# Optimization experiments

Measured on AMD Instinct MI355X. Metric: run time of the kernel, lower is better.

Reference implementation:

```python
import jax, jax.numpy as jnp
import numpy as np

HID = 64
NUM_LAYERS = 2
EPS = 1e-5


def _layernorm(x, g, b):
    mu = jnp.mean(x, axis=-1, keepdims=True)
    var = jnp.mean(jnp.square(x - mu), axis=-1, keepdims=True)
    return (x - mu) * jax.lax.rsqrt(var + EPS) * g + b


def _mlp(x, w1, b1, g, beta, w2, b2):
    # Linear -> LayerNorm -> ReLU -> Linear (torch Linear: x @ W.T + b)
    h = x @ w1.T + b1
    h = jax.nn.relu(_layernorm(h, g, beta))
    return h @ w2.T + b2


def _gru(x, h, wih, whh, bih, bhh):
    # PyTorch GRUCell semantics
    gi = x @ wih.T + bih
    gh = h @ whh.T + bhh
    ir, iz, inn = jnp.split(gi, 3, axis=-1)
    hr, hz, hn = jnp.split(gh, 3, axis=-1)
    r = jax.nn.sigmoid(ir + hr)
    z = jax.nn.sigmoid(iz + hz)
    n = jnp.tanh(inn + r * hn)
    return (1.0 - z) * n + z * h


def setup_inputs() -> dict:
    key = jax.random.key(0)
    ks = iter(jax.random.split(key, 64))
    s = 0.05

    def rn(shape):
        return jax.random.normal(next(ks), shape, dtype=jnp.float32) * s

    B, M, K1 = 32, 256, 128
    inp = {
        'hybrid_input': jax.random.normal(next(ks), (B, M, K1, 4), dtype=jnp.float32),
        'hidden_state': jnp.zeros((B, HID), dtype=jnp.float32),
        # input encoder
        'enc_w1': rn((HID, 4)), 'enc_b1': rn((HID,)),
        'enc_g': jnp.ones((HID,), jnp.float32), 'enc_beta': jnp.zeros((HID,), jnp.float32),
        'enc_w2': rn((HID, HID)), 'enc_b2': rn((HID,)),
        # per-layer, per-side (axis0=layer, axis1=[row,col]) params
        'l_w1': rn((NUM_LAYERS, 2, HID, HID)), 'l_b1': rn((NUM_LAYERS, 2, HID)),
        'l_g': jnp.ones((NUM_LAYERS, 2, HID), jnp.float32), 'l_beta': jnp.zeros((NUM_LAYERS, 2, HID), jnp.float32),
        'l_w2': rn((NUM_LAYERS, 2, HID, HID)), 'l_b2': rn((NUM_LAYERS, 2, HID)),
        'l_gwih': rn((NUM_LAYERS, 2, 3 * HID, HID)), 'l_gwhh': rn((NUM_LAYERS, 2, 3 * HID, HID)),
        'l_gbih': rn((NUM_LAYERS, 2, 3 * HID)), 'l_gbhh': rn((NUM_LAYERS, 2, 3 * HID)),
        # top-level GRU
        'g_wih': rn((3 * HID, HID)), 'g_whh': rn((3 * HID, HID)),
        'g_bih': rn((3 * HID,)), 'g_bhh': rn((3 * HID,)),
        # head: Linear(2H->H) -> ReLU -> Linear(H->1)
        'head_w1': rn((HID, 2 * HID)), 'head_b1': rn((HID,)),
        'head_w2': rn((1, HID)), 'head_b2': rn((1,)),
    }
    return inp


def reference(hybrid_input, hidden_state, enc_w1, enc_b1, enc_g, enc_beta, enc_w2, enc_b2,
              l_w1, l_b1, l_g, l_beta, l_w2, l_b2, l_gwih, l_gwhh, l_gbih, l_gbhh,
              g_wih, g_whh, g_bih, g_bhh, head_w1, head_b1, head_w2, head_b2):
    # input encoder
    x = _mlp(hybrid_input, enc_w1, enc_b1, enc_g, enc_beta, enc_w2, enc_b2)

    for l in range(NUM_LAYERS):
        # row pass: max over axis 2 (K+1)
        row_max = jnp.max(x, axis=2, keepdims=True)
        upd = _mlp(x - row_max, l_w1[l, 0], l_b1[l, 0], l_g[l, 0], l_beta[l, 0], l_w2[l, 0], l_b2[l, 0])
        x = _gru(upd, x, l_gwih[l, 0], l_gwhh[l, 0], l_gbih[l, 0], l_gbhh[l, 0])
        # col pass: max over axis 1 (M)
        col_max = jnp.max(x, axis=1, keepdims=True)
        upd = _mlp(x - col_max, l_w1[l, 1], l_b1[l, 1], l_g[l, 1], l_beta[l, 1], l_w2[l, 1], l_b2[l, 1])
        x = _gru(upd, x, l_gwih[l, 1], l_gwhh[l, 1], l_gbih[l, 1], l_gbhh[l, 1])

    B, M, K1, h = x.shape
    global_feat = jnp.max(x.reshape(B, M * K1, h), axis=1)  # (B, H)
    new_hidden = _gru(global_feat, hidden_state, g_wih, g_whh, g_bih, g_bhh)

    h_exp = jnp.broadcast_to(new_hidden[:, None, None, :], (B, M, K1, h))
    combined = jnp.concatenate([x, h_exp], axis=-1)  # (B, M, K1, 2H)
    hh = jax.nn.relu(combined @ head_w1.T + head_b1)
    logits = (hh @ head_w2.T + head_b2)[..., 0]  # (B, M, K1)
    return logits, new_hidden
```

## Files before the change

kernel.cpp:

```cpp
#include <hip/hip_runtime.h>
#include <math.h>

typedef unsigned int u32;
typedef unsigned short u16;
typedef __attribute__((ext_vector_type(4))) float f32x4;
typedef __attribute__((ext_vector_type(8))) short s16x8;

#define NTOT 1048576
#define SWZ(n, col) ((col) ^ (((n) & 7) << 4))

__device__ __forceinline__ float bflo(u32 v) { return __uint_as_float(v << 16); }
__device__ __forceinline__ float bfhi(u32 v) { return __uint_as_float(v & 0xffff0000u); }
__device__ __forceinline__ u16 f2bf(float f) {
  u32 u = __float_as_uint(f);
  u32 r = ((u >> 16) & 1u) + 0x7fffu;
  return (u16)((u + r) >> 16);
}
__device__ __forceinline__ u32 pk2(float a, float b) {
  return (u32)f2bf(a) | ((u32)f2bf(b) << 16);
}
__device__ __forceinline__ float sigm(float x) {
  return __builtin_amdgcn_rcpf(1.0f + __expf(-x));
}
__device__ __forceinline__ float tanh_f(float x) {
  float e = __expf(2.0f * x);
  return 1.0f - 2.0f * __builtin_amdgcn_rcpf(e + 1.0f);
}
__device__ __forceinline__ float relu(float x) { return fmaxf(x, 0.0f); }

__device__ __forceinline__ void gemmG(const ushort* __restrict__ gA,
                                      const unsigned char* L, int boff,
                                      int ws, int l, int lq, int lr,
                                      f32x4 acc[4]) {
  s16x8 a0 = *(const s16x8*)(gA + ((ws * 128 + l) << 3));
  s16x8 a1 = *(const s16x8*)(gA + ((ws * 128 + 64 + l) << 3));
  const int c0 = (lq << 4) ^ ((lr & 7) << 4);
  const unsigned char* Bp = L + boff + lr * 128;
#pragma unroll
  for (int nt = 0; nt < 4; ++nt) {
    s16x8 b0 = *(const s16x8*)(Bp + nt * 2048 + c0);
    s16x8 b1 = *(const s16x8*)(Bp + nt * 2048 + (c0 ^ 64));
    acc[nt] = __builtin_amdgcn_mfma_f32_16x16x32_bf16(a0, b0, acc[nt], 0, 0, 0);
    acc[nt] = __builtin_amdgcn_mfma_f32_16x16x32_bf16(a1, b1, acc[nt], 0, 0, 0);
  }
}

__device__ __forceinline__ void gemmG2(const ushort* __restrict__ gA,
                                       const unsigned char* L, int boff,
                                       int ws, int nh, int l, int lq, int lr,
                                       f32x4 acc[4]) {
  s16x8 a0 = *(const s16x8*)(gA + ((ws * 128 + l) << 3));
  s16x8 a1 = *(const s16x8*)(gA + ((ws * 128 + 64 + l) << 3));
  const int c0 = (lq << 4) ^ ((lr & 7) << 4);
  const unsigned char* Bp = L + boff + nh * 8192 + lr * 128;
#pragma unroll
  for (int nt = 0; nt < 4; ++nt) {
    s16x8 b0 = *(const s16x8*)(Bp + nt * 2048 + c0);
    s16x8 b1 = *(const s16x8*)(Bp + nt * 2048 + (c0 ^ 64));
    acc[nt] = __builtin_amdgcn_mfma_f32_16x16x32_bf16(a0, b0, acc[nt], 0, 0, 0);
    acc[nt] = __builtin_amdgcn_mfma_f32_16x16x32_bf16(a1, b1, acc[nt], 0, 0, 0);
  }
}

__device__ __forceinline__ void binit(f32x4 acc[4], float x, float y, float z, float w) {
  f32x4 v; v[0] = x; v[1] = y; v[2] = z; v[3] = w;
#pragma unroll
  for (int nt = 0; nt < 4; ++nt) acc[nt] = v;
}

__global__ void diag_kernel(float* out, float v) { out[0] = v; }

__global__ __launch_bounds__(256) void prep_kernel(
    const float* __restrict__ enc_w2, const float* __restrict__ head_w1,
    const float* __restrict__ l_w1, const float* __restrict__ l_w2,
    const float* __restrict__ l_gwih, const float* __restrict__ l_gwhh,
    ushort* __restrict__ gwF) {
  const int id = blockIdx.x;
  const int t = threadIdx.x;
  const float* src;
  int ld = 64;
  if (id == 0)      { src = enc_w2; }
  else if (id == 1) { src = head_w1; ld = 128; }
  else if (id < 6)  { src = l_w1 + (id - 2) * 4096; }
  else if (id < 10) { src = l_w2 + (id - 6) * 4096; }
  else if (id < 22) { int q = id - 10; src = l_gwih + (q / 3) * 12288 + (q % 3) * 4096; }
  else              { int q = id - 22; src = l_gwhh + (q / 3) * 12288 + (q % 3) * 4096; }
  uint4* dst = (uint4*)(gwF + (size_t)id * 4096);
#pragma unroll
  for (int i = 0; i < 2; ++i) {
    int ch = i * 256 + t;
    int q = ch & 63;
    int g = ch >> 6;
    int j = (g >> 1) * 16 + (q & 15);
    int k = (g & 1) * 32 + (q >> 4) * 8;
    const float* s = src + (size_t)j * ld + k;
    float4 f0 = *(const float4*)(s);
    float4 f1 = *(const float4*)(s + 4);
    uint4 o;
    o.x = pk2(f0.x, f0.y); o.y = pk2(f0.z, f0.w);
    o.z = pk2(f1.x, f1.y); o.w = pk2(f1.z, f1.w);
    dst[ch] = o;
  }
}

__global__ __launch_bounds__(512) void encoder_kernel(
    const float4* __restrict__ hyb, ushort* __restrict__ xG,
    const ushort* __restrict__ gwF, const float* __restrict__ enc_w1,
    const float* __restrict__ b1, const float* __restrict__ gg,
    const float* __restrict__ be, const float* __restrict__ b2,
    float* __restrict__ rmOut) {
  __shared__ __align__(16) unsigned char L[34304];
  const int t = threadIdx.x;
  const int w = t >> 6, l = t & 63, lq = l >> 4, lr = l & 15;
  const int ws = w & 3, nh = w >> 2;
  const int gbase = blockIdx.x * 128;
  const int j0 = ws * 16 + lq * 4;
  const int colb = ws * 32 + lq * 8;

  if (t < 256) ((float*)(L + 32768))[t] = enc_w1[t];
  __syncthreads();

  {
    const int n = t >> 2, part = t & 3;
    float4 iv = hyb[gbase + n];
    const float* W1 = (const float*)(L + 32768);
    float h[16];
#pragma unroll
    for (int jj = 0; jj < 16; ++jj) {
      int j = part * 16 + jj;
      float4 wr = *(const float4*)(W1 + j * 4);
      h[jj] = b1[j] + wr.x * iv.x + wr.y * iv.y + wr.z * iv.z + wr.w * iv.w;
    }
    float s = 0.f, q = 0.f;
#pragma unroll
    for (int jj = 0; jj < 16; ++jj) { s += h[jj]; q += h[jj] * h[jj]; }
    s += __shfl_xor(s, 1); q += __shfl_xor(q, 1);
    s += __shfl_xor(s, 2); q += __shfl_xor(q, 2);
    float mean = s * (1.f / 64.f);
    float rstd = rsqrtf(q * (1.f / 64.f) - mean * mean + 1e-5f);
    u32 pk[8];
#pragma unroll
    for (int jj = 0; jj < 16; jj += 2) {
      int j = part * 16 + jj;
      float v0 = relu((h[jj] - mean) * rstd * gg[j] + be[j]);
      float v1 = relu((h[jj + 1] - mean) * rstd * gg[j + 1] + be[j + 1]);
      pk[jj >> 1] = pk2(v0, v1);
    }
    *(uint4*)(L + n * 128 + SWZ(n, part * 32))      = make_uint4(pk[0], pk[1], pk[2], pk[3]);
    *(uint4*)(L + n * 128 + SWZ(n, part * 32 + 16)) = make_uint4(pk[4], pk[5], pk[6], pk[7]);
  }
  __syncthreads();

  float4 vb2 = *(const float4*)(b2 + j0);
  f32x4 acc[4];
  binit(acc, vb2.x, vb2.y, vb2.z, vb2.w);
  gemmG2(gwF, L, 0, ws, nh, l, lq, lr, acc);
#pragma unroll
  for (int nt = 0; nt < 4; ++nt) {
    int n = nh * 64 + nt * 16 + lr;
    *(uint2*)(L + 16384 + n * 128 + SWZ(n, colb)) =
        make_uint2(pk2(acc[nt][0], acc[nt][1]), pk2(acc[nt][2], acc[nt][3]));
  }
  {
    float mt[4];
#pragma unroll
    for (int r = 0; r < 4; ++r)
      mt[r] = fmaxf(fmaxf(acc[0][r], acc[1][r]), fmaxf(acc[2][r], acc[3][r]));
#pragma unroll
    for (int m = 1; m < 16; m <<= 1)
#pragma unroll
      for (int r = 0; r < 4; ++r) mt[r] = fmaxf(mt[r], __shfl_xor(mt[r], m));
    if (lr == 0) {
      float4 v; v.x = mt[0]; v.y = mt[1]; v.z = mt[2]; v.w = mt[3];
      *(float4*)(L + 33792 + (nh * 64 + j0) * 4) = v;
    }
  }
  __syncthreads();
  {
    uint4* xout = (uint4*)(xG + (size_t)gbase * 64);
#pragma unroll
    for (int i = 0; i < 2; ++i) {
      int flat = i * 512 + t; int n = flat >> 3, c = flat & 7;
      xout[(size_t)n * 8 + c] = *(const uint4*)(L + 16384 + n * 128 + SWZ(n, c * 16));
    }
  }
  if (t < 64) {
    const float* R = (const float*)(L + 33792);
    float v = fmaxf(R[t], R[64 + t]);
    rmOut[(size_t)(blockIdx.x * 2 + 0) * 64 + t] = v;
    rmOut[(size_t)(blockIdx.x * 2 + 1) * 64 + t] = v;
  }
}

#define PXL 0
#define PP  8192
#define PRED 16384

__global__ __launch_bounds__(256, 4) void pass_kernel(
    ushort* __restrict__ xG, const ushort* __restrict__ gwF,
    const float* __restrict__ rmP, const float* __restrict__ cmG, int mode,
    int s_w1, int s_w2, int s_ih0, int s_hh0,
    const float* __restrict__ b1, const float* __restrict__ b2,
    const float* __restrict__ gg, const float* __restrict__ be,
    const float* __restrict__ bih, const float* __restrict__ bhh,
    float* __restrict__ rmOut) {
  __shared__ __align__(16) unsigned char L[18432];
  const int t = threadIdx.x;
  const int ws = t >> 6, l = t & 63, lq = l >> 4, lr = l & 15;
  const int gbase = blockIdx.x * 64;
  const int j0 = ws * 16 + lq * 4;
  const int colb = ws * 32 + lq * 8;
  const int rowp = (gbase >> 7) * 2;
  const int b = gbase >> 15;
  const int k1b = gbase & 127;

  const ushort* Aw1 = gwF + (size_t)s_w1 * 4096;
  const ushort* Aw2 = gwF + (size_t)s_w2 * 4096;
  const ushort* Ai0 = gwF + (size_t)s_ih0 * 4096;
  const ushort* Ai1 = Ai0 + 4096;
  const ushort* Ai2 = Ai1 + 4096;
  const ushort* Ah0 = gwF + (size_t)s_hh0 * 4096;
  const ushort* Ah1 = Ah0 + 4096;
  const ushort* Ah2 = Ah1 + 4096;

  {
    const uint4* xrow = (const uint4*)(xG + (size_t)gbase * 64);
#pragma unroll
    for (int i = 0; i < 2; ++i) {
      int flat = i * 256 + t; int n = flat >> 3, c = flat & 7;
      uint4 xv = xrow[(size_t)n * 8 + c];
      *(uint4*)(L + PXL + n * 128 + SWZ(n, c * 16)) = xv;
      float mv[8];
      if (mode == 0) {
        const float* r0 = rmP + (size_t)rowp * 64 + c * 8;
#pragma unroll
        for (int q = 0; q < 8; ++q) mv[q] = fmaxf(r0[q], r0[64 + q]);
      } else {
        const float* cp = cmG + ((size_t)(b * 128 + k1b + n)) * 64 + c * 8;
#pragma unroll
        for (int q = 0; q < 8; ++q) mv[q] = cp[q];
      }
      uint4 o;
      o.x = pk2(bflo(xv.x) - mv[0], bfhi(xv.x) - mv[1]);
      o.y = pk2(bflo(xv.y) - mv[2], bfhi(xv.y) - mv[3]);
      o.z = pk2(bflo(xv.z) - mv[4], bfhi(xv.z) - mv[5]);
      o.w = pk2(bflo(xv.w) - mv[6], bfhi(xv.w) - mv[7]);
      *(uint4*)(L + PP + n * 128 + SWZ(n, c * 16)) = o;
    }
  }
  __syncthreads();

  f32x4 acc[4];
  { float4 v = *(const float4*)(b1 + j0); binit(acc, v.x, v.y, v.z, v.w); }
  gemmG(Aw1, L, PP, ws, l, lq, lr, acc);
#pragma unroll
  for (int nt = 0; nt < 4; ++nt) {
    float s = acc[nt][0] + acc[nt][1] + acc[nt][2] + acc[nt][3];
    float q = acc[nt][0] * acc[nt][0] + acc[nt][1] * acc[nt][1] +
              acc[nt][2] * acc[nt][2] + acc[nt][3] * acc[nt][3];
    s += __shfl_xor(s, 16); q += __shfl_xor(q, 16);
    s += __shfl_xor(s, 32); q += __shfl_xor(q, 32);
    if (lq == 0)
      *(float2*)(L + PRED + (ws * 64 + nt * 16 + lr) * 8) = make_float2(s, q);
  }
  __syncthreads();
  {
    float4 vg = *(const float4*)(gg + j0);
    float4 vbe = *(const float4*)(be + j0);
    float gv[4] = {vg.x, vg.y, vg.z, vg.w};
    float bv[4] = {vbe.x, vbe.y, vbe.z, vbe.w};
#pragma unroll
    for (int nt = 0; nt < 4; ++nt) {
      int np = nt * 16 + lr;
      float ss = 0.f, qq = 0.f;
#pragma unroll
      for (int wv = 0; wv < 4; ++wv) {
        float2 pr = *(const float2*)(L + PRED + (wv * 64 + np) * 8);
        ss += pr.x; qq += pr.y;
      }
      float mean = ss * (1.f / 64.f);
      float rstd = rsqrtf(qq * (1.f / 64.f) - mean * mean + 1e-5f);
      float h_[4];
#pragma unroll
      for (int r = 0; r < 4; ++r) h_[r] = relu((acc[nt][r] - mean) * rstd * gv[r] + bv[r]);
      *(uint2*)(L + PP + np * 128 + SWZ(np, colb)) =
          make_uint2(pk2(h_[0], h_[1]), pk2(h_[2], h_[3]));
    }
  }
  __syncthreads();
  __builtin_amdgcn_sched_barrier(0);

  { float4 v = *(const float4*)(b2 + j0); binit(acc, v.x, v.y, v.z, v.w); }
  gemmG(Aw2, L, PP, ws, l, lq, lr, acc);
  __syncthreads();
#pragma unroll
  for (int nt = 0; nt < 4; ++nt) {
    int n = nt * 16 + lr;
    *(uint2*)(L + PP + n * 128 + SWZ(n, colb)) =
        make_uint2(pk2(acc[nt][0], acc[nt][1]), pk2(acc[nt][2], acc[nt][3]));
  }
  __syncthreads();
  __builtin_amdgcn_sched_barrier(0);

  f32x4 ah[4];
  { float4 v = *(const float4*)(bhh + 128 + j0); binit(ah, v.x, v.y, v.z, v.w); }
  gemmG(Ah2, L, PXL, ws, l, lq, lr, ah);
  __builtin_amdgcn_sched_barrier(0);

  f32x4 ar[4];
  { float4 vi = *(const float4*)(bih + j0);
    float4 vh = *(const float4*)(bhh + j0);
    binit(ar, vi.x + vh.x, vi.y + vh.y, vi.z + vh.z, vi.w + vh.w); }
  gemmG(Ai0, L, PP, ws, l, lq, lr, ar);
  gemmG(Ah0, L, PXL, ws, l, lq, lr, ar);
  __builtin_amdgcn_sched_barrier(0);

  f32x4 an[4];
  { float4 v = *(const float4*)(bih + 128 + j0);
    float bv[4] = {v.x, v.y, v.z, v.w};
#pragma unroll
    for (int nt = 0; nt < 4; ++nt)
#pragma unroll
      for (int r = 0; r < 4; ++r)
        an[nt][r] = bv[r] + sigm(ar[nt][r]) * ah[nt][r];
  }
  gemmG(Ai2, L, PP, ws, l, lq, lr, an);
  __builtin_amdgcn_sched_barrier(0);

  f32x4 az[4];
  { float4 vi = *(const float4*)(bih + 64 + j0);
    float4 vh = *(const float4*)(bhh + 64 + j0);
    binit(az, vi.x + vh.x, vi.y + vh.y, vi.z + vh.z, vi.w + vh.w); }
  gemmG(Ai1, L, PP, ws, l, lq, lr, az);
  gemmG(Ah1, L, PXL, ws, l, lq, lr, az);

  float xn[4][4];
#pragma unroll
  for (int nt = 0; nt < 4; ++nt) {
    int n = nt * 16 + lr;
    uint2 xo = *(const uint2*)(L + PXL + n * 128 + SWZ(n, colb));
    float xv[4] = {bflo(xo.x), bfhi(xo.x), bflo(xo.y), bfhi(xo.y)};
#pragma unroll
    for (int r = 0; r < 4; ++r) {
      float nn = tanh_f(an[nt][r]);
      float zz = sigm(az[nt][r]);
      xn[nt][r] = nn + zz * (xv[r] - nn);
    }
  }
  __syncthreads();
#pragma unroll
  for (int nt = 0; nt < 4; ++nt) {
    int n = nt * 16 + lr;
    *(uint2*)(L + PXL + n * 128 + SWZ(n, colb)) =
        make_uint2(pk2(xn[nt][0], xn[nt][1]), pk2(xn[nt][2], xn[nt][3]));
  }
  {
    float mt[4];
#pragma unroll
    for (int r = 0; r < 4; ++r)
      mt[r] = fmaxf(fmaxf(xn[0][r], xn[1][r]), fmaxf(xn[2][r], xn[3][r]));
#pragma unroll
    for (int m = 1; m < 16; m <<= 1)
#pragma unroll
      for (int r = 0; r < 4; ++r) mt[r] = fmaxf(mt[r], __shfl_xor(mt[r], m));
    if (lr == 0) {
      float4 v; v.x = mt[0]; v.y = mt[1]; v.z = mt[2]; v.w = mt[3];
      *(float4*)(rmOut + (size_t)blockIdx.x * 64 + j0) = v;
    }
  }
  __syncthreads();
  {
    uint4* xout = (uint4*)(xG + (size_t)gbase * 64);
#pragma unroll
    for (int i = 0; i < 2; ++i) {
      int flat = i * 256 + t; int n = flat >> 3, c = flat & 7;
      xout[(size_t)n * 8 + c] = *(const uint4*)(L + PXL + n * 128 + SWZ(n, c * 16));
    }
  }
}

__global__ __launch_bounds__(256) void colmax_kernel(const ushort* __restrict__ xG,
                                                     float* __restrict__ cm) {
  const int t = threadIdx.x;
  const int b = blockIdx.x >> 4, kg = blockIdx.x & 15;
  const int col = t & 31, k1 = kg * 8 + (t >> 5);
  const u32* xu = (const u32*)xG;
  float m0 = -INFINITY, m1 = -INFINITY;
  for (int m = 0; m < 256; ++m) {
    size_t node = ((size_t)(b * 256 + m)) * 128 + k1;
    u32 v = xu[node * 32 + col];
    m0 = fmaxf(m0, bflo(v)); m1 = fmaxf(m1, bfhi(v));
  }
  float* dst = cm + ((size_t)(b * 128 + k1)) * 64 + col * 2;
  dst[0] = m0; dst[1] = m1;
}

__global__ __launch_bounds__(64) void topgru_kernel(
    const float* __restrict__ rm, const float* __restrict__ hs,
    const float* __restrict__ gwih, const float* __restrict__ gwhh,
    const float* __restrict__ gbih, const float* __restrict__ gbhh,
    float* __restrict__ nh, float* __restrict__ outTail) {
  __shared__ float gf[64], h0[64];
  const int b = blockIdx.x, j = threadIdx.x;
  float g0 = -INFINITY, g1 = -INFINITY, g2 = -INFINITY, g3 = -INFINITY;
  const float* base = rm + (size_t)b * 512 * 64 + j;
  for (int r = 0; r < 512; r += 4) {
    g0 = fmaxf(g0, base[(r + 0) * 64]);
    g1 = fmaxf(g1, base[(r + 1) * 64]);
    g2 = fmaxf(g2, base[(r + 2) * 64]);
    g3 = fmaxf(g3, base[(r + 3) * 64]);
  }
  gf[j] = fmaxf(fmaxf(g0, g1), fmaxf(g2, g3));
  h0[j] = hs[b * 64 + j];
  __syncthreads();
  float gi[3], gh[3];
#pragma unroll
  for (int g = 0; g < 3; ++g) {
    float s = gbih[g * 64 + j];
    const float* wr = gwih + (g * 64 + j) * 64;
    for (int k = 0; k < 64; ++k) s += wr[k] * gf[k];
    gi[g] = s;
  }
#pragma unroll
  for (int g = 0; g < 3; ++g) {
    float s = gbhh[g * 64 + j];
    const float* wr = gwhh + (g * 64 + j) * 64;
    for (int k = 0; k < 64; ++k) s += wr[k] * h0[k];
    gh[g] = s;
  }
  float rr = sigm(gi[0] + gh[0]);
  float zz = sigm(gi[1] + gh[1]);
  float nn = tanh_f(gi[2] + rr * gh[2]);
  float val = (1.0f - zz) * nn + zz * h0[j];
  nh[b * 64 + j] = val;
  outTail[b * 64 + j] = val;
}

__global__ __launch_bounds__(64) void hc_kernel(const float* __restrict__ nh,
                                                const float* __restrict__ hw1,
                                                const float* __restrict__ hb1,
                                                float* __restrict__ hc) {
  __shared__ float h0[64];
  const int b = blockIdx.x, j = threadIdx.x;
  h0[j] = nh[b * 64 + j];
  __syncthreads();
  float s = hb1[j];
  const float* wr = hw1 + j * 128 + 64;
  for (int k = 0; k < 64; ++k) s += wr[k] * h0[k];
  hc[b * 64 + j] = s;
}

__global__ __launch_bounds__(512) void head_kernel(
    const ushort* __restrict__ xG, const ushort* __restrict__ gwF,
    const float* __restrict__ hc, const float* __restrict__ hw2,
    const float* __restrict__ hb2, float* __restrict__ out) {
  __shared__ __align__(16) unsigned char L[18432];
  const int t = threadIdx.x;
  const int w = t >> 6, l = t & 63, lq = l >> 4, lr = l & 15;
  const int ws = w & 3, nh = w >> 2;
  const int gbase = blockIdx.x * 128;
  const int b = gbase >> 15;
  const int j0 = ws * 16 + lq * 4;

  { const uint4* xrow = (const uint4*)(xG + (size_t)gbase * 64);
#pragma unroll
    for (int i = 0; i < 2; ++i) {
      int flat = i * 512 + t; int n = flat >> 3, c = flat & 7;
      *(uint4*)(L + n * 128 + SWZ(n, c * 16)) = xrow[(size_t)n * 8 + c];
    } }
  __syncthreads();

  float4 vhc = *(const float4*)(hc + b * 64 + j0);
  f32x4 acc[4];
  binit(acc, vhc.x, vhc.y, vhc.z, vhc.w);
  gemmG2(gwF + 4096, L, 0, ws, nh, l, lq, lr, acc);

  float4 w2v = *(const float4*)(hw2 + j0);
  float w2a[4] = {w2v.x, w2v.y, w2v.z, w2v.w};
#pragma unroll
  for (int nt = 0; nt < 4; ++nt) {
    float p = 0.f;
#pragma unroll
    for (int r = 0; r < 4; ++r) p += w2a[r] * relu(acc[nt][r]);
    p += __shfl_xor(p, 16);
    p += __shfl_xor(p, 32);
    if (lq == 0) ((float*)(L + 16384))[(nh * 4 + ws) * 64 + nt * 16 + lr] = p;
  }
  __syncthreads();
  if (t < 128) {
    const float* red = (const float*)(L + 16384) + (t >> 6) * 256 + (t & 63);
    out[gbase + t] = red[0] + red[64] + red[128] + red[192] + hb2[0];
  }
}

extern "C" void kernel_launch(void* const* d_in, const int* in_sizes, int n_in,
                              void* d_out, int out_size, void* d_ws, size_t ws_size,
                              hipStream_t stream) {
  const float* hybrid   = (const float*)d_in[0];
  const float* hidden   = (const float*)d_in[1];
  const float* enc_w1   = (const float*)d_in[2];
  const float* enc_b1   = (const float*)d_in[3];
  const float* enc_g    = (const float*)d_in[4];
  const float* enc_beta = (const float*)d_in[5];
  const float* enc_w2   = (const float*)d_in[6];
  const float* enc_b2   = (const float*)d_in[7];
  const float* l_w1     = (const float*)d_in[8];
  const float* l_b1     = (const float*)d_in[9];
  const float* l_g      = (const float*)d_in[10];
  const float* l_beta   = (const float*)d_in[11];
  const float* l_w2     = (const float*)d_in[12];
  const float* l_b2     = (const float*)d_in[13];
  const float* l_gwih   = (const float*)d_in[14];
  const float* l_gwhh   = (const float*)d_in[15];
  const float* l_gbih   = (const float*)d_in[16];
  const float* l_gbhh   = (const float*)d_in[17];
  const float* g_wih    = (const float*)d_in[18];
  const float* g_whh    = (const float*)d_in[19];
  const float* g_bih    = (const float*)d_in[20];
  const float* g_bhh    = (const float*)d_in[21];
  const float* head_w1  = (const float*)d_in[22];
  const float* head_b1  = (const float*)d_in[23];
  const float* head_w2  = (const float*)d_in[24];
  const float* head_b2  = (const float*)d_in[25];

  char* p = (char*)d_ws;
  size_t off = 0;
  auto carve = [&](size_t bytes) { void* r = p + off; off = (off + bytes + 255) & ~255ULL; return r; };
  ushort* xG  = (ushort*)carve((size_t)NTOT * 64 * 2);
  ushort* gwF = (ushort*)carve(34 * 4096 * 2);
  float*  rmA = (float*)carve((size_t)16384 * 64 * 4);
  float*  rmB = (float*)carve((size_t)16384 * 64 * 4);
  float*  cmG = (float*)carve((size_t)32 * 128 * 64 * 4);
  float*  nh  = (float*)carve(2048 * 4);
  float*  hcb = (float*)carve(2048 * 4);

  if (ws_size < off) {
    diag_kernel<<<1, 1, 0, stream>>>((float*)d_out, 1.0f + (float)ws_size * 1e-9f);
    return;
  }

  prep_kernel<<<34, 256, 0, stream>>>(enc_w2, head_w1, l_w1, l_w2, l_gwih, l_gwhh, gwF);
  encoder_kernel<<<8192, 512, 0, stream>>>((const float4*)hybrid, xG, gwF, enc_w1,
                                           enc_b1, enc_g, enc_beta, enc_b2, rmA);

  float* rmRead = rmA;
  float* rmWrite = rmB;
  for (int lyr = 0; lyr < 2; ++lyr) {
    for (int s = 0; s < 2; ++s) {
      const int m = lyr * 2 + s;
      if (s == 1) colmax_kernel<<<512, 256, 0, stream>>>(xG, cmG);
      pass_kernel<<<16384, 256, 0, stream>>>(
          xG, gwF, rmRead, cmG, s,
          2 + m, 6 + m, 10 + 3 * m, 22 + 3 * m,
          l_b1 + m * 64, l_b2 + m * 64, l_g + m * 64, l_beta + m * 64,
          l_gbih + m * 192, l_gbhh + m * 192, rmWrite);
      float* tmp = rmRead; rmRead = rmWrite; rmWrite = tmp;
    }
  }

  topgru_kernel<<<32, 64, 0, stream>>>(rmRead, hidden, g_wih, g_whh, g_bih, g_bhh,
                                       nh, (float*)d_out + 1048576);
  hc_kernel<<<32, 64, 0, stream>>>(nh, head_w1, head_b1, hcb);
  head_kernel<<<8192, 512, 0, stream>>>(xG, gwF, hcb, head_w2, head_b2, (float*)d_out);
}
```

Measured before the change: 749.1 us.

## Write outputs directly to global, add separate LDS buffer to drop barriers

The pass and encoder kernels now store their bf16 results straight from registers to global memory as 8-byte writes. Before, results were staged through LDS and copied out as 16-byte coalesced stores. The MLP output in pass_kernel goes to a new LDS region, so it no longer overwrites the hidden buffer, and several __syncthreads are removed. LDS grows and launch bounds rise to 5 blocks per CU. bf16 packing uses a v_perm byte permute. The risk is less coalesced global stores in exchange for fewer barriers and LDS round trips.

```diff
diff --git a/kernel.cpp b/kernel.cpp
--- a/kernel.cpp
+++ b/kernel.cpp
@@ -11,13 +11,12 @@
 
 __device__ __forceinline__ float bflo(u32 v) { return __uint_as_float(v << 16); }
 __device__ __forceinline__ float bfhi(u32 v) { return __uint_as_float(v & 0xffff0000u); }
-__device__ __forceinline__ u16 f2bf(float f) {
+__device__ __forceinline__ u32 rndbf(float f) {
   u32 u = __float_as_uint(f);
-  u32 r = ((u >> 16) & 1u) + 0x7fffu;
-  return (u16)((u + r) >> 16);
+  return u + 0x7fffu + ((u >> 16) & 1u);
 }
 __device__ __forceinline__ u32 pk2(float a, float b) {
-  return (u32)f2bf(a) | ((u32)f2bf(b) << 16);
+  return __builtin_amdgcn_perm(rndbf(b), rndbf(a), 0x07060302u);
 }
 __device__ __forceinline__ float sigm(float x) {
   return __builtin_amdgcn_rcpf(1.0f + __expf(-x));
@@ -155,11 +154,14 @@
   f32x4 acc[4];
   binit(acc, vb2.x, vb2.y, vb2.z, vb2.w);
   gemmG2(gwF, L, 0, ws, nh, l, lq, lr, acc);
-#pragma unroll
-  for (int nt = 0; nt < 4; ++nt) {
-    int n = nh * 64 + nt * 16 + lr;
-    *(uint2*)(L + 16384 + n * 128 + SWZ(n, colb)) =
-        make_uint2(pk2(acc[nt][0], acc[nt][1]), pk2(acc[nt][2], acc[nt][3]));
+  {
+    ushort* xout = xG + (size_t)gbase * 64;
+#pragma unroll
+    for (int nt = 0; nt < 4; ++nt) {
+      int n = nh * 64 + nt * 16 + lr;
+      *(uint2*)(xout + (size_t)n * 64 + j0) =
+          make_uint2(pk2(acc[nt][0], acc[nt][1]), pk2(acc[nt][2], acc[nt][3]));
+    }
   }
   {
     float mt[4];
@@ -176,14 +178,6 @@
     }
   }
   __syncthreads();
-  {
-    uint4* xout = (uint4*)(xG + (size_t)gbase * 64);
-#pragma unroll
-    for (int i = 0; i < 2; ++i) {
-      int flat = i * 512 + t; int n = flat >> 3, c = flat & 7;
-      xout[(size_t)n * 8 + c] = *(const uint4*)(L + 16384 + n * 128 + SWZ(n, c * 16));
-    }
-  }
   if (t < 64) {
     const float* R = (const float*)(L + 33792);
     float v = fmaxf(R[t], R[64 + t]);
@@ -194,9 +188,10 @@
 
 #define PXL 0
 #define PP  8192
-#define PRED 16384
-
-__global__ __launch_bounds__(256, 4) void pass_kernel(
+#define PU  16384
+#define PRED 24576
+
+__global__ __launch_bounds__(256, 5) void pass_kernel(
     ushort* __restrict__ xG, const ushort* __restrict__ gwF,
     const float* __restrict__ rmP, const float* __restrict__ cmG, int mode,
     int s_w1, int s_w2, int s_ih0, int s_hh0,
@@ -204,7 +199,7 @@
     const float* __restrict__ gg, const float* __restrict__ be,
     const float* __restrict__ bih, const float* __restrict__ bhh,
     float* __restrict__ rmOut) {
-  __shared__ __align__(16) unsigned char L[18432];
+  __shared__ __align__(16) unsigned char L[26624];
   const int t = threadIdx.x;
   const int ws = t >> 6, l = t & 63, lq = l >> 4, lr = l & 15;
   const int gbase = blockIdx.x * 64;
@@ -292,26 +287,25 @@
 
   { float4 v = *(const float4*)(b2 + j0); binit(acc, v.x, v.y, v.z, v.w); }
   gemmG(Aw2, L, PP, ws, l, lq, lr, acc);
-  __syncthreads();
 #pragma unroll
   for (int nt = 0; nt < 4; ++nt) {
     int n = nt * 16 + lr;
-    *(uint2*)(L + PP + n * 128 + SWZ(n, colb)) =
+    *(uint2*)(L + PU + n * 128 + SWZ(n, colb)) =
         make_uint2(pk2(acc[nt][0], acc[nt][1]), pk2(acc[nt][2], acc[nt][3]));
   }
-  __syncthreads();
   __builtin_amdgcn_sched_barrier(0);
 
   f32x4 ah[4];
   { float4 v = *(const float4*)(bhh + 128 + j0); binit(ah, v.x, v.y, v.z, v.w); }
   gemmG(Ah2, L, PXL, ws, l, lq, lr, ah);
+  __syncthreads();
   __builtin_amdgcn_sched_barrier(0);
 
   f32x4 ar[4];
   { float4 vi = *(const float4*)(bih + j0);
     float4 vh = *(const float4*)(bhh + j0);
     binit(ar, vi.x + vh.x, vi.y + vh.y, vi.z + vh.z, vi.w + vh.w); }
-  gemmG(Ai0, L, PP, ws, l, lq, lr, ar);
+  gemmG(Ai0, L, PU, ws, l, lq, lr, ar);
   gemmG(Ah0, L, PXL, ws, l, lq, lr, ar);
   __builtin_amdgcn_sched_barrier(0);
 
@@ -324,14 +318,14 @@
       for (int r = 0; r < 4; ++r)
         an[nt][r] = bv[r] + sigm(ar[nt][r]) * ah[nt][r];
   }
-  gemmG(Ai2, L, PP, ws, l, lq, lr, an);
+  gemmG(Ai2, L, PU, ws, l, lq, lr, an);
   __builtin_amdgcn_sched_barrier(0);
 
   f32x4 az[4];
   { float4 vi = *(const float4*)(bih + 64 + j0);
     float4 vh = *(const float4*)(bhh + 64 + j0);
     binit(az, vi.x + vh.x, vi.y + vh.y, vi.z + vh.z, vi.w + vh.w); }
-  gemmG(Ai1, L, PP, ws, l, lq, lr, az);
+  gemmG(Ai1, L, PU, ws, l, lq, lr, az);
   gemmG(Ah1, L, PXL, ws, l, lq, lr, az);
 
   float xn[4][4];
@@ -347,12 +341,14 @@
       xn[nt][r] = nn + zz * (xv[r] - nn);
     }
   }
-  __syncthreads();
-#pragma unroll
-  for (int nt = 0; nt < 4; ++nt) {
-    int n = nt * 16 + lr;
-    *(uint2*)(L + PXL + n * 128 + SWZ(n, colb)) =
-        make_uint2(pk2(xn[nt][0], xn[nt][1]), pk2(xn[nt][2], xn[nt][3]));
+  {
+    ushort* xout = xG + (size_t)gbase * 64;
+#pragma unroll
+    for (int nt = 0; nt < 4; ++nt) {
+      int n = nt * 16 + lr;
+      *(uint2*)(xout + (size_t)n * 64 + j0) =
+          make_uint2(pk2(xn[nt][0], xn[nt][1]), pk2(xn[nt][2], xn[nt][3]));
+    }
   }
   {
     float mt[4];
@@ -366,15 +362,6 @@
     if (lr == 0) {
       float4 v; v.x = mt[0]; v.y = mt[1]; v.z = mt[2]; v.w = mt[3];
       *(float4*)(rmOut + (size_t)blockIdx.x * 64 + j0) = v;
-    }
-  }
-  __syncthreads();
-  {
-    uint4* xout = (uint4*)(xG + (size_t)gbase * 64);
-#pragma unroll
-    for (int i = 0; i < 2; ++i) {
-      int flat = i * 256 + t; int n = flat >> 3, c = flat & 7;
-      xout[(size_t)n * 8 + c] = *(const uint4*)(L + PXL + n * 128 + SWZ(n, c * 16));
     }
   }
 }
```

Result: no change. 762.5 us (+1.8%).
